# Kernel tuning notes

Measured on AMD Instinct MI355X. Metric: run time of the kernel, lower is better.

Reference implementation:

```python
import jax, jax.numpy as jnp
import numpy as np

NEG_SLOPE = 0.2
RECON_W = 0.1
BN_EPS = 1e-5


def gat_conv(x, edge_index, W, a_src, a_dst, b):
    """PyG-style GATConv (eval mode, add_self_loops=True, concat heads).
    x: [N, F_in], W: [F_in, H*C], a_src/a_dst: [H, C], b: [H*C]."""
    N = x.shape[0]
    H, C = a_src.shape
    h = (x @ W).reshape(N, H, C)                      # [N,H,C]
    loop = jnp.arange(N, dtype=edge_index.dtype)
    src = jnp.concatenate([edge_index[0], loop])
    dst = jnp.concatenate([edge_index[1], loop])
    alpha_src = jnp.sum(h * a_src, axis=-1)           # [N,H]
    alpha_dst = jnp.sum(h * a_dst, axis=-1)           # [N,H]
    e = jax.nn.leaky_relu(alpha_src[src] + alpha_dst[dst], NEG_SLOPE)  # [E,H]
    # segment softmax over incoming edges of each destination node
    m = jax.ops.segment_max(e, dst, num_segments=N)
    e = jnp.exp(e - m[dst])
    s = jax.ops.segment_sum(e, dst, num_segments=N)
    p = e / s[dst]                                    # [E,H]
    out = jax.ops.segment_sum(p[:, :, None] * h[src], dst, num_segments=N)  # [N,H,C]
    return out.reshape(N, H * C) + b


def setup_inputs() -> dict:
    key = jax.random.key(0)
    ks = jax.random.split(key, 24)
    N, E = 100000, 800000
    F_in, hid, heads, n_cls, ctx_d, expl_d = 128, 32, 4, 10, 6, 32
    HC = hid * heads  # 128
    g = lambda k, shp, sc=0.1: jax.random.normal(k, shp, dtype=jnp.float32) * sc
    return {
        "x": jax.random.normal(ks[0], (N, F_in), dtype=jnp.float32),
        "edge_index": jax.random.randint(ks[1], (2, E), 0, N, dtype=jnp.int32),
        "context": jax.random.normal(ks[2], (N, ctx_d), dtype=jnp.float32),
        # GATConv 1: F_in -> hid, heads
        "W1": g(ks[3], (F_in, HC)), "a_src1": g(ks[4], (heads, hid)),
        "a_dst1": g(ks[5], (heads, hid)), "b1": g(ks[6], (HC,)),
        # BatchNorm1d(HC), eval mode
        "bn_gamma": jnp.ones((HC,), jnp.float32), "bn_beta": g(ks[7], (HC,)),
        "bn_mean": g(ks[8], (HC,)), "bn_var": jax.random.uniform(ks[9], (HC,), jnp.float32, 0.5, 1.5),
        # GATConv 2: HC -> hid, 1 head
        "W2": g(ks[10], (HC, hid)), "a_src2": g(ks[11], (1, hid)),
        "a_dst2": g(ks[12], (1, hid)), "b2": g(ks[13], (hid,)),
        # Reasoner MLP: ctx_d -> hid -> expl_d
        "rw1": g(ks[14], (ctx_d, hid)), "rb1": g(ks[15], (hid,)),
        "rw2": g(ks[16], (hid, expl_d)), "rb2": g(ks[17], (expl_d,)),
        # Decoder: expl_d -> hid
        "dw": g(ks[18], (expl_d, hid)), "db": g(ks[19], (hid,)),
        # Classifier: hid -> n_cls
        "cw": g(ks[20], (hid, n_cls)), "cb": g(ks[21], (n_cls,)),
    }


def reference(x, edge_index, context, W1, a_src1, a_dst1, b1,
              bn_gamma, bn_beta, bn_mean, bn_var,
              W2, a_src2, a_dst2, b2, rw1, rb1, rw2, rb2, dw, db, cw, cb):
    # layer 1: GAT -> BN(eval) -> ELU (dropout inactive in eval)
    h = gat_conv(x, edge_index, W1, a_src1, a_dst1, b1)
    h = (h - bn_mean) * jax.lax.rsqrt(bn_var + BN_EPS) * bn_gamma + bn_beta
    h = jax.nn.elu(h)
    # layer 2: GAT (1 head)
    h = gat_conv(h, edge_index, W2, a_src2, a_dst2, b2)  # [N, hid]
    # reasoner + decoder
    expl = jnp.maximum(context @ rw1 + rb1, 0.0) @ rw2 + rb2   # [N, expl_d]
    recon = expl @ dw + db                                     # [N, hid]
    combined = h + RECON_W * recon
    logits = combined @ cw + cb
    return jax.nn.log_softmax(logits, axis=1), expl
```

## Files before the change

kernel.cpp:

```cpp
#include <hip/hip_runtime.h>
#include <hip/hip_bf16.h>
#include <math.h>

#define NEG_SLOPE 0.2f
#define RECON_W 0.1f
#define BN_EPS 1e-5f
#define CAP 64
#define NB_SCAT 256

typedef __attribute__((ext_vector_type(8))) short short8;
typedef __attribute__((ext_vector_type(4))) float f32x4;

__device__ __forceinline__ float lrelu(float v) {
    return (v >= 0.f) ? v : NEG_SLOPE * v;
}
__device__ __forceinline__ unsigned short f2bf(float f) {
    unsigned int u = __float_as_uint(f);
    u = (u + 0x7fffu + ((u >> 16) & 1u)) >> 16;
    return (unsigned short)u;
}
__device__ __forceinline__ float bf2f(unsigned short u) {
    return __uint_as_float(((unsigned int)u) << 16);
}
__device__ __forceinline__ unsigned int pack2bf(float a, float b) {
    return (unsigned int)f2bf(a) | ((unsigned int)f2bf(b) << 16);
}
__device__ __forceinline__ void unpack2(unsigned int u, float& a, float& b) {
    a = bf2f((unsigned short)u);
    b = bf2f((unsigned short)(u >> 16));
}

__global__ __launch_bounds__(256) void prep_kernel(
    const float* __restrict__ W1, const float* __restrict__ W2,
    const float* __restrict__ b1, const float* __restrict__ g,
    const float* __restrict__ be, const float* __restrict__ m, const float* __restrict__ v,
    unsigned short* __restrict__ w1t, unsigned short* __restrict__ w2t,
    float* __restrict__ bnsc, float* __restrict__ bnsh) {
    int b = blockIdx.x, tid = threadIdx.x;
    if (b < 64) {
        int e = b * 256 + tid;
        w1t[e] = f2bf(W1[(e & 127) * 128 + (e >> 7)]);
    } else {
        #pragma unroll
        for (int it = 0; it < 16; it++) {
            int e = it * 256 + tid;
            w2t[e] = f2bf(W2[(e & 127) * 32 + (e >> 7)]);
        }
        if (tid < 128) {
            float s = rsqrtf(v[tid] + BN_EPS) * g[tid];
            bnsc[tid] = s;
            bnsh[tid] = (b1[tid] - m[tid]) * s + be[tid];
        }
    }
}

__global__ __launch_bounds__(256) void gemm1_mfma_kernel(
    const float* __restrict__ x, const unsigned short* __restrict__ w1t,
    const float* __restrict__ a_src, const float* __restrict__ a_dst,
    unsigned short* __restrict__ h1g, float* __restrict__ as1, float* __restrict__ ad1, int N,
    const int* __restrict__ esrc, const int* __restrict__ edst, int E,
    int* __restrict__ cnt, int* __restrict__ csrS) {
    __shared__ unsigned short sA[64 * 128];
    __shared__ unsigned short sBt[128 * 128];
    __shared__ float s_as[128], s_ad[128];
    int tid = threadIdx.x;

    if (blockIdx.x < NB_SCAT) {
        int stride = NB_SCAT * 256;
        #pragma unroll 2
        for (int e = blockIdx.x * 256 + tid; e < E; e += stride) {
            int s = esrc[e], d = edst[e];
            int pos = atomicAdd(&cnt[d], 1);
            if (pos < CAP) csrS[(size_t)d * CAP + pos] = s;
        }
        return;
    }
    int rowBase = (blockIdx.x - NB_SCAT) * 64;

    if (tid < 128) { s_as[tid] = a_src[tid]; s_ad[tid] = a_dst[tid]; }
    #pragma unroll
    for (int u = 0; u < 8; u++) {
        int f = tid + u * 256;
        int r = f >> 5, cg = f & 31;
        int gr = rowBase + r;
        float4 vv = make_float4(0.f, 0.f, 0.f, 0.f);
        if (gr < N) vv = *(const float4*)(x + (size_t)gr * 128 + cg * 4);
        uint2 pk;
        pk.x = pack2bf(vv.x, vv.y);
        pk.y = pack2bf(vv.z, vv.w);
        ((uint2*)sA)[f] = pk;
    }
    #pragma unroll
    for (int u = 0; u < 8; u++) {
        int f = tid + u * 256;
        ((uint4*)sBt)[f] = ((const uint4*)w1t)[f];
    }
    __syncthreads();

    int lane = tid & 63;
    int w = tid >> 6;
    int quad = lane >> 4;
    int m16 = lane & 15;

    f32x4 acc[8];
    #pragma unroll
    for (int t = 0; t < 8; t++) acc[t] = (f32x4){0.f, 0.f, 0.f, 0.f};

    #pragma unroll
    for (int kc = 0; kc < 4; kc++) {
        int k0 = kc * 32 + quad * 8;
        short8 af = *(const short8*)(sA + ((w * 16 + m16) * 128 + k0));
        #pragma unroll
        for (int t = 0; t < 8; t++) {
            short8 bf = *(const short8*)(sBt + ((t * 16 + m16) * 128 + k0));
            acc[t] = __builtin_amdgcn_mfma_f32_16x16x32_bf16(af, bf, acc[t], 0, 0, 0);
        }
    }

    #pragma unroll
    for (int t = 0; t < 8; t++) {
        #pragma unroll
        for (int r = 0; r < 4; r++) {
            int row = w * 16 + quad * 4 + r;
            int col = t * 16 + m16;
            sA[row * 128 + col] = f2bf(acc[t][r]);
        }
    }
    __syncthreads();
    #pragma unroll
    for (int u = 0; u < 8; u++) {
        int f = tid + u * 256;
        int r = f >> 5, cg = f & 31;
        int gr = rowBase + r;
        if (gr < N) *(uint2*)(h1g + (size_t)gr * 128 + cg * 4) = ((const uint2*)sA)[f];
    }
    {
        int row = tid >> 2, head = tid & 3;
        int gr = rowBase + row;
        if (gr < N) {
            const unsigned int* rowp = (const unsigned int*)(sA + row * 128);
            float ps = 0.f, pd = 0.f;
            #pragma unroll
            for (int j = 0; j < 16; j++) {
                float f0, f1;
                unpack2(rowp[head * 16 + j], f0, f1);
                int c = head * 32 + j * 2;
                ps = fmaf(f0, s_as[c], fmaf(f1, s_as[c + 1], ps));
                pd = fmaf(f0, s_ad[c], fmaf(f1, s_ad[c + 1], pd));
            }
            as1[gr * 4 + head] = ps;
            ad1[gr * 4 + head] = pd;
        }
    }
}

__global__ __launch_bounds__(256) void agg1_gemm2_kernel(
    const unsigned short* __restrict__ h1g,
    const float* __restrict__ as1, const float* __restrict__ ad1,
    const int* __restrict__ cnt, const int* __restrict__ csrS,
    const float* __restrict__ bnscale, const float* __restrict__ bnshift,
    const unsigned short* __restrict__ w2t,
    const float* __restrict__ a_src2, const float* __restrict__ a_dst2,
    unsigned short* __restrict__ h2g, float* __restrict__ as2, float* __restrict__ ad2,
    int N) {
    __shared__ int   sSrc[16][CAP + 1];
    __shared__ __align__(16) float sW[16][CAP + 1][4];
    __shared__ unsigned short sH[16 * 128];
    __shared__ float s_as[32], s_ad[32];
    int tid = threadIdx.x;
    int nid = tid >> 4;
    int l   = tid & 15;
    int n = blockIdx.x * 16 + nid;
    bool alive = (n < N);
    int total = 0;

    if (tid < 32) { s_as[tid] = a_src2[tid]; s_ad[tid] = a_dst2[tid]; }

    if (alive) {
        int deg = min(cnt[n], CAP);
        total = deg + 1;
        float4 ad4 = *(const float4*)(ad1 + (size_t)n * 4);
        for (int slot = l; slot < total; slot += 16) {
            int s = (slot < deg) ? csrS[(size_t)n * CAP + slot] : n;
            sSrc[nid][slot] = s;
            float4 a = *(const float4*)(as1 + (size_t)s * 4);
            float4 w4;
            w4.x = __expf(lrelu(a.x + ad4.x));
            w4.y = __expf(lrelu(a.y + ad4.y));
            w4.z = __expf(lrelu(a.z + ad4.z));
            w4.w = __expf(lrelu(a.w + ad4.w));
            *(float4*)(&sW[nid][slot][0]) = w4;
        }
    }
    __syncthreads();

    int hl = l >> 2;
    unsigned choff = (unsigned)(l << 3);
    const int* sS = sSrc[nid];
    const float* sWp = &sW[nid][0][0];

    float pa0 = 0.f, pa1 = 0.f, pa2 = 0.f, pa3 = 0.f;
    float pa4 = 0.f, pa5 = 0.f, pa6 = 0.f, pa7 = 0.f;
    float pb0 = 0.f, pb1 = 0.f, pb2 = 0.f, pb3 = 0.f;
    float pb4 = 0.f, pb5 = 0.f, pb6 = 0.f, pb7 = 0.f;
    float sa = 0.f, sb = 0.f;
    int j = 0;
    for (; j + 1 < total; j += 2) {
        int s0 = sS[j];
        int s1 = sS[j + 1];
        float w0 = sWp[(j << 2) + hl];
        float w1 = sWp[((j + 1) << 2) + hl];
        uint4 u0 = *(const uint4*)(h1g + (((unsigned)s0 << 7) + choff));
        uint4 u1 = *(const uint4*)(h1g + (((unsigned)s1 << 7) + choff));
        float f0, f1;
        unpack2(u0.x, f0, f1); pa0 = fmaf(w0, f0, pa0); pa1 = fmaf(w0, f1, pa1);
        unpack2(u0.y, f0, f1); pa2 = fmaf(w0, f0, pa2); pa3 = fmaf(w0, f1, pa3);
        unpack2(u0.z, f0, f1); pa4 = fmaf(w0, f0, pa4); pa5 = fmaf(w0, f1, pa5);
        unpack2(u0.w, f0, f1); pa6 = fmaf(w0, f0, pa6); pa7 = fmaf(w0, f1, pa7);
        sa += w0;
        unpack2(u1.x, f0, f1); pb0 = fmaf(w1, f0, pb0); pb1 = fmaf(w1, f1, pb1);
        unpack2(u1.y, f0, f1); pb2 = fmaf(w1, f0, pb2); pb3 = fmaf(w1, f1, pb3);
        unpack2(u1.z, f0, f1); pb4 = fmaf(w1, f0, pb4); pb5 = fmaf(w1, f1, pb5);
        unpack2(u1.w, f0, f1); pb6 = fmaf(w1, f0, pb6); pb7 = fmaf(w1, f1, pb7);
        sb += w1;
    }
    if (j < total) {
        int s0 = sS[j];
        float w0 = sWp[(j << 2) + hl];
        uint4 u0 = *(const uint4*)(h1g + (((unsigned)s0 << 7) + choff));
        float f0, f1;
        unpack2(u0.x, f0, f1); pa0 = fmaf(w0, f0, pa0); pa1 = fmaf(w0, f1, pa1);
        unpack2(u0.y, f0, f1); pa2 = fmaf(w0, f0, pa2); pa3 = fmaf(w0, f1, pa3);
        unpack2(u0.z, f0, f1); pa4 = fmaf(w0, f0, pa4); pa5 = fmaf(w0, f1, pa5);
        unpack2(u0.w, f0, f1); pa6 = fmaf(w0, f0, pa6); pa7 = fmaf(w0, f1, pa7);
        sa += w0;
    }
    uint4 pk = make_uint4(0u, 0u, 0u, 0u);
    if (alive) {
        float inv = 1.f / (sa + sb);
        float4 sc0 = *(const float4*)(bnscale + l * 8);
        float4 sc1 = *(const float4*)(bnscale + l * 8 + 4);
        float4 sh0 = *(const float4*)(bnshift + l * 8);
        float4 sh1 = *(const float4*)(bnshift + l * 8 + 4);
        float o0 = fmaf((pa0 + pb0) * inv, sc0.x, sh0.x);
        float o1 = fmaf((pa1 + pb1) * inv, sc0.y, sh0.y);
        float o2 = fmaf((pa2 + pb2) * inv, sc0.z, sh0.z);
        float o3 = fmaf((pa3 + pb3) * inv, sc0.w, sh0.w);
        float o4 = fmaf((pa4 + pb4) * inv, sc1.x, sh1.x);
        float o5 = fmaf((pa5 + pb5) * inv, sc1.y, sh1.y);
        float o6 = fmaf((pa6 + pb6) * inv, sc1.z, sh1.z);
        float o7 = fmaf((pa7 + pb7) * inv, sc1.w, sh1.w);
        o0 = (o0 > 0.f) ? o0 : expm1f(o0);
        o1 = (o1 > 0.f) ? o1 : expm1f(o1);
        o2 = (o2 > 0.f) ? o2 : expm1f(o2);
        o3 = (o3 > 0.f) ? o3 : expm1f(o3);
        o4 = (o4 > 0.f) ? o4 : expm1f(o4);
        o5 = (o5 > 0.f) ? o5 : expm1f(o5);
        o6 = (o6 > 0.f) ? o6 : expm1f(o6);
        o7 = (o7 > 0.f) ? o7 : expm1f(o7);
        pk.x = pack2bf(o0, o1);
        pk.y = pack2bf(o2, o3);
        pk.z = pack2bf(o4, o5);
        pk.w = pack2bf(o6, o7);
    }
    *(uint4*)(sH + nid * 128 + l * 8) = pk;
    __syncthreads();

    unsigned short* sBt = (unsigned short*)&sW[0][0][0];
    unsigned short* sC  = sBt + 32 * 128;
    #pragma unroll
    for (int u = 0; u < 2; u++) ((uint4*)sBt)[tid + u * 256] = ((const uint4*)w2t)[tid + u * 256];
    __syncthreads();

    if (tid < 64) {
        int quad = tid >> 4, m16 = tid & 15;
        f32x4 acc2[2];
        acc2[0] = (f32x4){0.f, 0.f, 0.f, 0.f};
        acc2[1] = (f32x4){0.f, 0.f, 0.f, 0.f};
        #pragma unroll
        for (int kc = 0; kc < 4; kc++) {
            int k0 = kc * 32 + quad * 8;
            short8 af = *(const short8*)(sH + m16 * 128 + k0);
            #pragma unroll
            for (int t = 0; t < 2; t++) {
                short8 bf = *(const short8*)(sBt + (t * 16 + m16) * 128 + k0);
                acc2[t] = __builtin_amdgcn_mfma_f32_16x16x32_bf16(af, bf, acc2[t], 0, 0, 0);
            }
        }
        #pragma unroll
        for (int t = 0; t < 2; t++) {
            #pragma unroll
            for (int r = 0; r < 4; r++) {
                sC[(quad * 4 + r) * 32 + t * 16 + m16] = f2bf(acc2[t][r]);
            }
        }
    }
    __syncthreads();

    if (tid < 64) {
        int row = tid >> 2, g = tid & 3;
        int gr = blockIdx.x * 16 + row;
        if (gr < N) *(uint4*)(h2g + (size_t)gr * 32 + g * 8) = ((const uint4*)sC)[tid];
    }
    if (tid >= 64 && tid < 80) {
        int row = tid - 64;
        int gr = blockIdx.x * 16 + row;
        if (gr < N) {
            const unsigned int* rowp = (const unsigned int*)(sC + row * 32);
            float ps = 0.f, pd = 0.f;
            #pragma unroll
            for (int jj = 0; jj < 16; jj++) {
                float f0, f1;
                unpack2(rowp[jj], f0, f1);
                ps = fmaf(f0, s_as[jj * 2], fmaf(f1, s_as[jj * 2 + 1], ps));
                pd = fmaf(f0, s_ad[jj * 2], fmaf(f1, s_ad[jj * 2 + 1], pd));
            }
            as2[gr] = ps;
            ad2[gr] = pd;
        }
    }
}

__global__ __launch_bounds__(256) void agg2_head_kernel(
    const unsigned short* __restrict__ h2g,
    const float* __restrict__ as2, const float* __restrict__ ad2,
    const int* __restrict__ cnt, const int* __restrict__ csrS,
    const float* __restrict__ b2, const float* __restrict__ context,
    const float* __restrict__ rw1, const float* __restrict__ rb1,
    const float* __restrict__ rw2, const float* __restrict__ rb2,
    const float* __restrict__ dw, const float* __restrict__ db,
    const float* __restrict__ cw, const float* __restrict__ cb,
    float* __restrict__ out_lsm, float* __restrict__ out_expl, int N) {
    __shared__ int   sSrc[32][CAP + 1];
    __shared__ __align__(16) float sW[32][CAP + 1];
    __shared__ float sHL[32][32];
    __shared__ float s_rw1[192], s_rw2[1024], s_dw[1024], s_cw[320];
    __shared__ float s_rb1[32], s_rb2[32], s_db[32], s_b2[32], s_cb[16];
    int tid = threadIdx.x;
    for (int i = tid; i < 1024; i += 256) { s_rw2[i] = rw2[i]; s_dw[i] = dw[i]; }
    for (int i = tid; i < 320; i += 256) s_cw[i] = cw[i];
    if (tid < 192) s_rw1[tid] = rw1[tid];
    if (tid < 32) { s_rb1[tid] = rb1[tid]; s_rb2[tid] = rb2[tid]; s_db[tid] = db[tid]; s_b2[tid] = b2[tid]; }
    if (tid < 10) s_cb[tid] = cb[tid];

    int nid = tid >> 3;
    int l   = tid & 7;
    int n = blockIdx.x * 32 + nid;
    bool alive = (n < N);
    int total = 0;

    if (alive) {
        int deg = min(cnt[n], CAP);
        total = deg + 1;
        float ad = ad2[n];
        for (int slot = l; slot < total; slot += 8) {
            int s = (slot < deg) ? csrS[(size_t)n * CAP + slot] : n;
            sSrc[nid][slot] = s;
            sW[nid][slot] = __expf(lrelu(as2[s] + ad));
        }
    }
    __syncthreads();

    unsigned choff = (unsigned)(l << 2);
    const int* sS = sSrc[nid];
    const float* sWp = &sW[nid][0];

    float a0a = 0.f, a1a = 0.f, a2a = 0.f, a3a = 0.f, sa = 0.f;
    float a0b = 0.f, a1b = 0.f, a2b = 0.f, a3b = 0.f, sb = 0.f;
    int j = 0;
    for (; j + 1 < total; j += 2) {
        int s0 = sS[j];
        int s1 = sS[j + 1];
        float w0 = sWp[j];
        float w1 = sWp[j + 1];
        uint2 u0 = *(const uint2*)(h2g + (((unsigned)s0 << 5) + choff));
        uint2 u1 = *(const uint2*)(h2g + (((unsigned)s1 << 5) + choff));
        float f0, f1;
        unpack2(u0.x, f0, f1); a0a = fmaf(w0, f0, a0a); a1a = fmaf(w0, f1, a1a);
        unpack2(u0.y, f0, f1); a2a = fmaf(w0, f0, a2a); a3a = fmaf(w0, f1, a3a);
        sa += w0;
        unpack2(u1.x, f0, f1); a0b = fmaf(w1, f0, a0b); a1b = fmaf(w1, f1, a1b);
        unpack2(u1.y, f0, f1); a2b = fmaf(w1, f0, a2b); a3b = fmaf(w1, f1, a3b);
        sb += w1;
    }
    if (j < total) {
        int s0 = sS[j];
        float w0 = sWp[j];
        uint2 u0 = *(const uint2*)(h2g + (((unsigned)s0 << 5) + choff));
        float f0, f1;
        unpack2(u0.x, f0, f1); a0a = fmaf(w0, f0, a0a); a1a = fmaf(w0, f1, a1a);
        unpack2(u0.y, f0, f1); a2a = fmaf(w0, f0, a2a); a3a = fmaf(w0, f1, a3a);
        sa += w0;
    }
    if (alive) {
        float inv = 1.f / (sa + sb);
        int c0 = l * 4;
        sHL[nid][c0 + 0] = (a0a + a0b) * inv + s_b2[c0 + 0];
        sHL[nid][c0 + 1] = (a1a + a1b) * inv + s_b2[c0 + 1];
        sHL[nid][c0 + 2] = (a2a + a2b) * inv + s_b2[c0 + 2];
        sHL[nid][c0 + 3] = (a3a + a3b) * inv + s_b2[c0 + 3];
    }
    __syncthreads();

    float* sEX = &sW[0][0];

    if (alive) {
        int c0 = l * 4;
        float ctxv[6];
        #pragma unroll
        for (int i = 0; i < 6; i++) ctxv[i] = context[(size_t)n * 6 + i];
        float t1[32];
        #pragma unroll
        for (int c = 0; c < 32; c++) t1[c] = s_rb1[c];
        #pragma unroll
        for (int i = 0; i < 6; i++) {
            float s = ctxv[i];
            #pragma unroll
            for (int c = 0; c < 32; c++) t1[c] = fmaf(s, s_rw1[i * 32 + c], t1[c]);
        }
        #pragma unroll
        for (int c = 0; c < 32; c++) t1[c] = fmaxf(t1[c], 0.f);

        float e0 = s_rb2[c0], e1 = s_rb2[c0 + 1], e2 = s_rb2[c0 + 2], e3 = s_rb2[c0 + 3];
        #pragma unroll
        for (int c = 0; c < 32; c++) {
            float s = t1[c];
            const float* rp = s_rw2 + c * 32 + c0;
            e0 = fmaf(s, rp[0], e0); e1 = fmaf(s, rp[1], e1);
            e2 = fmaf(s, rp[2], e2); e3 = fmaf(s, rp[3], e3);
        }
        *(float4*)(out_expl + (size_t)n * 32 + c0) = make_float4(e0, e1, e2, e3);
        sEX[nid * 32 + c0 + 0] = e0;
        sEX[nid * 32 + c0 + 1] = e1;
        sEX[nid * 32 + c0 + 2] = e2;
        sEX[nid * 32 + c0 + 3] = e3;
    }
    __syncthreads();

    if (alive) {
        int c0 = l * 4;
        float r0 = s_db[c0], r1 = s_db[c0 + 1], r2 = s_db[c0 + 2], r3 = s_db[c0 + 3];
        #pragma unroll
        for (int c = 0; c < 32; c++) {
            float s = sEX[nid * 32 + c];
            const float* dp = s_dw + c * 32 + c0;
            r0 = fmaf(s, dp[0], r0); r1 = fmaf(s, dp[1], r1);
            r2 = fmaf(s, dp[2], r2); r3 = fmaf(s, dp[3], r3);
        }
        float cmb[4];
        cmb[0] = sHL[nid][c0 + 0] + RECON_W * r0;
        cmb[1] = sHL[nid][c0 + 1] + RECON_W * r1;
        cmb[2] = sHL[nid][c0 + 2] + RECON_W * r2;
        cmb[3] = sHL[nid][c0 + 3] + RECON_W * r3;
        float lg[10];
        #pragma unroll
        for (int c = 0; c < 10; c++) lg[c] = 0.f;
        #pragma unroll
        for (int k = 0; k < 4; k++) {
            float s = cmb[k];
            const float* cp = s_cw + (c0 + k) * 10;
            #pragma unroll
            for (int c = 0; c < 10; c++) lg[c] = fmaf(s, cp[c], lg[c]);
        }
        #pragma unroll
        for (int m = 1; m < 8; m <<= 1) {
            #pragma unroll
            for (int c = 0; c < 10; c++) lg[c] += __shfl_xor(lg[c], m);
        }
        #pragma unroll
        for (int c = 0; c < 10; c++) lg[c] += s_cb[c];
        float mx = lg[0];
        #pragma unroll
        for (int c = 1; c < 10; c++) mx = fmaxf(mx, lg[c]);
        float se = 0.f;
        #pragma unroll
        for (int c = 0; c < 10; c++) se += expf(lg[c] - mx);
        float lse = mx + logf(se);
        out_lsm[(size_t)n * 10 + l] = lg[l] - lse;
        if (l < 2) out_lsm[(size_t)n * 10 + 8 + l] = lg[8 + l] - lse;
    }
}

extern "C" void kernel_launch(void* const* d_in, const int* in_sizes, int n_in,
                              void* d_out, int out_size, void* d_ws, size_t ws_size,
                              hipStream_t stream) {
    const float* x    = (const float*)d_in[0];
    const int* ei     = (const int*)d_in[1];
    const float* ctx  = (const float*)d_in[2];
    const float* W1   = (const float*)d_in[3];
    const float* a_s1 = (const float*)d_in[4];
    const float* a_d1 = (const float*)d_in[5];
    const float* b1   = (const float*)d_in[6];
    const float* bn_g = (const float*)d_in[7];
    const float* bn_b = (const float*)d_in[8];
    const float* bn_m = (const float*)d_in[9];
    const float* bn_v = (const float*)d_in[10];
    const float* W2   = (const float*)d_in[11];
    const float* a_s2 = (const float*)d_in[12];
    const float* a_d2 = (const float*)d_in[13];
    const float* b2   = (const float*)d_in[14];
    const float* rw1  = (const float*)d_in[15];
    const float* rb1  = (const float*)d_in[16];
    const float* rw2  = (const float*)d_in[17];
    const float* rb2  = (const float*)d_in[18];
    const float* dw   = (const float*)d_in[19];
    const float* db   = (const float*)d_in[20];
    const float* cw   = (const float*)d_in[21];
    const float* cb   = (const float*)d_in[22];

    int N = in_sizes[0] / 128;
    int E = in_sizes[1] / 2;
    const int* esrc = ei;
    const int* edst = ei + E;

    char* w = (char*)d_ws;
    auto alloc = [&](size_t bytes) {
        void* p = (void*)w;
        w += (bytes + 255) & ~(size_t)255;
        return p;
    };
    unsigned short* h1g = (unsigned short*)alloc((size_t)N * 128 * 2);
    unsigned short* h2g = (unsigned short*)alloc((size_t)N * 32 * 2);
    float* as1  = (float*)alloc((size_t)N * 4 * 4);
    float* ad1  = (float*)alloc((size_t)N * 4 * 4);
    float* as2  = (float*)alloc((size_t)N * 4);
    float* ad2  = (float*)alloc((size_t)N * 4);
    int* cnt    = (int*)alloc((size_t)N * 4);
    int* csrS   = (int*)alloc((size_t)N * CAP * 4);
    float* bnsc = (float*)alloc(128 * 4);
    float* bnsh = (float*)alloc(128 * 4);
    unsigned short* w1t = (unsigned short*)alloc(128 * 128 * 2);
    unsigned short* w2t = (unsigned short*)alloc(32 * 128 * 2);

    float* out0 = (float*)d_out;
    float* out1 = out0 + (size_t)N * 10;

    hipMemsetAsync(cnt, 0, (size_t)N * 4, stream);

    prep_kernel<<<65, 256, 0, stream>>>(W1, W2, b1, bn_g, bn_b, bn_m, bn_v,
                                        w1t, w2t, bnsc, bnsh);
    gemm1_mfma_kernel<<<NB_SCAT + (N + 63) / 64, 256, 0, stream>>>(
        x, w1t, a_s1, a_d1, h1g, as1, ad1, N, esrc, edst, E, cnt, csrS);
    agg1_gemm2_kernel<<<(N + 15) / 16, 256, 0, stream>>>(
        h1g, as1, ad1, cnt, csrS, bnsc, bnsh, w2t, a_s2, a_d2, h2g, as2, ad2, N);
    agg2_head_kernel<<<(N + 31) / 32, 256, 0, stream>>>(
        h2g, as2, ad2, cnt, csrS, b2, ctx, rw1, rb1, rw2, rb2,
        dw, db, cw, cb, out0, out1, N);
}
```

Before: 272.5 us.

## Fuse memset, weight prep, and GEMM1/scatter into one cooperative persistent kernel

Replaces the memset, the prep kernel and the GEMM1+edge-scatter kernel with one cooperative kernel. It zeroes the counts, converts the weights and computes the BN constants, then runs a grid-wide sync. After the sync, a quarter of the blocks do the edge scatter and the rest loop persistently over 64-row GEMM tiles. This removes two launches and their gaps, but adds a grid barrier and a smaller persistent grid. The GEMM blocks now load the W1 tile once and reuse it across tiles, though each block may get less latency hiding than the old oversubscribed launch.

```diff
diff --git a/kernel.cpp b/kernel.cpp
--- a/kernel.cpp
+++ b/kernel.cpp
@@ -1,12 +1,14 @@
 #include <hip/hip_runtime.h>
+#include <hip/hip_cooperative_groups.h>
 #include <hip/hip_bf16.h>
 #include <math.h>
+
+namespace cg = cooperative_groups;
 
 #define NEG_SLOPE 0.2f
 #define RECON_W 0.1f
 #define BN_EPS 1e-5f
 #define CAP 64
-#define NB_SCAT 256
 
 typedef __attribute__((ext_vector_type(8))) short short8;
 typedef __attribute__((ext_vector_type(4))) float f32x4;
@@ -30,33 +32,14 @@
     b = bf2f((unsigned short)(u >> 16));
 }
 
-__global__ __launch_bounds__(256) void prep_kernel(
+__global__ __launch_bounds__(256) void fused1_kernel(
+    const float* __restrict__ x,
     const float* __restrict__ W1, const float* __restrict__ W2,
-    const float* __restrict__ b1, const float* __restrict__ g,
-    const float* __restrict__ be, const float* __restrict__ m, const float* __restrict__ v,
+    const float* __restrict__ b1, const float* __restrict__ bn_g,
+    const float* __restrict__ bn_b, const float* __restrict__ bn_m, const float* __restrict__ bn_v,
+    const float* __restrict__ a_src, const float* __restrict__ a_dst,
     unsigned short* __restrict__ w1t, unsigned short* __restrict__ w2t,
-    float* __restrict__ bnsc, float* __restrict__ bnsh) {
-    int b = blockIdx.x, tid = threadIdx.x;
-    if (b < 64) {
-        int e = b * 256 + tid;
-        w1t[e] = f2bf(W1[(e & 127) * 128 + (e >> 7)]);
-    } else {
-        #pragma unroll
-        for (int it = 0; it < 16; it++) {
-            int e = it * 256 + tid;
-            w2t[e] = f2bf(W2[(e & 127) * 32 + (e >> 7)]);
-        }
-        if (tid < 128) {
-            float s = rsqrtf(v[tid] + BN_EPS) * g[tid];
-            bnsc[tid] = s;
-            bnsh[tid] = (b1[tid] - m[tid]) * s + be[tid];
-        }
-    }
-}
-
-__global__ __launch_bounds__(256) void gemm1_mfma_kernel(
-    const float* __restrict__ x, const unsigned short* __restrict__ w1t,
-    const float* __restrict__ a_src, const float* __restrict__ a_dst,
+    float* __restrict__ bnsc, float* __restrict__ bnsh,
     unsigned short* __restrict__ h1g, float* __restrict__ as1, float* __restrict__ ad1, int N,
     const int* __restrict__ esrc, const int* __restrict__ edst, int E,
     int* __restrict__ cnt, int* __restrict__ csrS) {
@@ -64,9 +47,22 @@
     __shared__ unsigned short sBt[128 * 128];
     __shared__ float s_as[128], s_ad[128];
     int tid = threadIdx.x;
-
-    if (blockIdx.x < NB_SCAT) {
-        int stride = NB_SCAT * 256;
+    int T = gridDim.x * 256;
+    int gtid = blockIdx.x * 256 + tid;
+
+    for (int i = gtid; i < N; i += T) cnt[i] = 0;
+    for (int i = gtid; i < 16384; i += T) w1t[i] = f2bf(W1[(i & 127) * 128 + (i >> 7)]);
+    for (int i = gtid; i < 4096; i += T) w2t[i] = f2bf(W2[(i & 127) * 32 + (i >> 7)]);
+    for (int i = gtid; i < 128; i += T) {
+        float s = rsqrtf(bn_v[i] + BN_EPS) * bn_g[i];
+        bnsc[i] = s;
+        bnsh[i] = (b1[i] - bn_m[i]) * s + bn_b[i];
+    }
+    cg::this_grid().sync();
+
+    int nbs = gridDim.x >> 2;
+    if ((int)blockIdx.x < nbs) {
+        int stride = nbs * 256;
         #pragma unroll 2
         for (int e = blockIdx.x * 256 + tid; e < E; e += stride) {
             int s = esrc[e], d = edst[e];
@@ -75,81 +71,85 @@
         }
         return;
     }
-    int rowBase = (blockIdx.x - NB_SCAT) * 64;
 
     if (tid < 128) { s_as[tid] = a_src[tid]; s_ad[tid] = a_dst[tid]; }
     #pragma unroll
     for (int u = 0; u < 8; u++) {
         int f = tid + u * 256;
-        int r = f >> 5, cg = f & 31;
-        int gr = rowBase + r;
-        float4 vv = make_float4(0.f, 0.f, 0.f, 0.f);
-        if (gr < N) vv = *(const float4*)(x + (size_t)gr * 128 + cg * 4);
-        uint2 pk;
-        pk.x = pack2bf(vv.x, vv.y);
-        pk.y = pack2bf(vv.z, vv.w);
-        ((uint2*)sA)[f] = pk;
-    }
-    #pragma unroll
-    for (int u = 0; u < 8; u++) {
-        int f = tid + u * 256;
         ((uint4*)sBt)[f] = ((const uint4*)w1t)[f];
     }
-    __syncthreads();
 
     int lane = tid & 63;
     int w = tid >> 6;
     int quad = lane >> 4;
     int m16 = lane & 15;
-
-    f32x4 acc[8];
-    #pragma unroll
-    for (int t = 0; t < 8; t++) acc[t] = (f32x4){0.f, 0.f, 0.f, 0.f};
-
-    #pragma unroll
-    for (int kc = 0; kc < 4; kc++) {
-        int k0 = kc * 32 + quad * 8;
-        short8 af = *(const short8*)(sA + ((w * 16 + m16) * 128 + k0));
-        #pragma unroll
-        for (int t = 0; t < 8; t++) {
-            short8 bf = *(const short8*)(sBt + ((t * 16 + m16) * 128 + k0));
-            acc[t] = __builtin_amdgcn_mfma_f32_16x16x32_bf16(af, bf, acc[t], 0, 0, 0);
-        }
-    }
-
-    #pragma unroll
-    for (int t = 0; t < 8; t++) {
-        #pragma unroll
-        for (int r = 0; r < 4; r++) {
-            int row = w * 16 + quad * 4 + r;
-            int col = t * 16 + m16;
-            sA[row * 128 + col] = f2bf(acc[t][r]);
-        }
-    }
-    __syncthreads();
-    #pragma unroll
-    for (int u = 0; u < 8; u++) {
-        int f = tid + u * 256;
-        int r = f >> 5, cg = f & 31;
-        int gr = rowBase + r;
-        if (gr < N) *(uint2*)(h1g + (size_t)gr * 128 + cg * 4) = ((const uint2*)sA)[f];
-    }
-    {
-        int row = tid >> 2, head = tid & 3;
-        int gr = rowBase + row;
-        if (gr < N) {
-            const unsigned int* rowp = (const unsigned int*)(sA + row * 128);
-            float ps = 0.f, pd = 0.f;
-            #pragma unroll
-            for (int j = 0; j < 16; j++) {
-                float f0, f1;
-                unpack2(rowp[head * 16 + j], f0, f1);
-                int c = head * 32 + j * 2;
-                ps = fmaf(f0, s_as[c], fmaf(f1, s_as[c + 1], ps));
-                pd = fmaf(f0, s_ad[c], fmaf(f1, s_ad[c + 1], pd));
+    int nTiles = (N + 63) / 64;
+    int gstride = gridDim.x - nbs;
+
+    for (int t = (int)blockIdx.x - nbs; t < nTiles; t += gstride) {
+        __syncthreads();
+        int rowBase = t * 64;
+        #pragma unroll
+        for (int u = 0; u < 8; u++) {
+            int f = tid + u * 256;
+            int r = f >> 5, cg2 = f & 31;
+            int gr = rowBase + r;
+            float4 vv = make_float4(0.f, 0.f, 0.f, 0.f);
+            if (gr < N) vv = *(const float4*)(x + (size_t)gr * 128 + cg2 * 4);
+            uint2 pk;
+            pk.x = pack2bf(vv.x, vv.y);
+            pk.y = pack2bf(vv.z, vv.w);
+            ((uint2*)sA)[f] = pk;
+        }
+        __syncthreads();
+
+        f32x4 acc[8];
+        #pragma unroll
+        for (int tt = 0; tt < 8; tt++) acc[tt] = (f32x4){0.f, 0.f, 0.f, 0.f};
+        #pragma unroll
+        for (int kc = 0; kc < 4; kc++) {
+            int k0 = kc * 32 + quad * 8;
+            short8 af = *(const short8*)(sA + ((w * 16 + m16) * 128 + k0));
+            #pragma unroll
+            for (int tt = 0; tt < 8; tt++) {
+                short8 bf = *(const short8*)(sBt + ((tt * 16 + m16) * 128 + k0));
+                acc[tt] = __builtin_amdgcn_mfma_f32_16x16x32_bf16(af, bf, acc[tt], 0, 0, 0);
             }
-            as1[gr * 4 + head] = ps;
-            ad1[gr * 4 + head] = pd;
+        }
+        #pragma unroll
+        for (int tt = 0; tt < 8; tt++) {
+            #pragma unroll
+            for (int r = 0; r < 4; r++) {
+                int row = w * 16 + quad * 4 + r;
+                int col = tt * 16 + m16;
+                sA[row * 128 + col] = f2bf(acc[tt][r]);
+            }
+        }
+        __syncthreads();
+        #pragma unroll
+        for (int u = 0; u < 8; u++) {
+            int f = tid + u * 256;
+            int r = f >> 5, cg2 = f & 31;
+            int gr = rowBase + r;
+            if (gr < N) *(uint2*)(h1g + (size_t)gr * 128 + cg2 * 4) = ((const uint2*)sA)[f];
+        }
+        {
+            int row = tid >> 2, head = tid & 3;
+            int gr = rowBase + row;
+            if (gr < N) {
+                const unsigned int* rowp = (const unsigned int*)(sA + row * 128);
+                float ps = 0.f, pd = 0.f;
+                #pragma unroll
+                for (int j = 0; j < 16; j++) {
+                    float f0, f1;
+                    unpack2(rowp[head * 16 + j], f0, f1);
+                    int c = head * 32 + j * 2;
+                    ps = fmaf(f0, s_as[c], fmaf(f1, s_as[c + 1], ps));
+                    pd = fmaf(f0, s_ad[c], fmaf(f1, s_ad[c + 1], pd));
+                }
+                as1[gr * 4 + head] = ps;
+                ad1[gr * 4 + head] = pd;
+            }
         }
     }
 }
@@ -535,12 +535,26 @@
     float* out0 = (float*)d_out;
     float* out1 = out0 + (size_t)N * 10;
 
-    hipMemsetAsync(cnt, 0, (size_t)N * 4, stream);
-
-    prep_kernel<<<65, 256, 0, stream>>>(W1, W2, b1, bn_g, bn_b, bn_m, bn_v,
-                                        w1t, w2t, bnsc, bnsh);
-    gemm1_mfma_kernel<<<NB_SCAT + (N + 63) / 64, 256, 0, stream>>>(
-        x, w1t, a_s1, a_d1, h1g, as1, ad1, N, esrc, edst, E, cnt, csrS);
+    int maxBpc = 0;
+    if (hipOccupancyMaxActiveBlocksPerMultiprocessor(
+            &maxBpc, (const void*)fused1_kernel, 256, 0) != hipSuccess || maxBpc <= 0) {
+        maxBpc = 2;
+    }
+    if (maxBpc > 3) maxBpc = 3;
+    int coopGrid = maxBpc * 256;
+
+    void* args[] = {
+        (void*)&x, (void*)&W1, (void*)&W2,
+        (void*)&b1, (void*)&bn_g, (void*)&bn_b, (void*)&bn_m, (void*)&bn_v,
+        (void*)&a_s1, (void*)&a_d1,
+        (void*)&w1t, (void*)&w2t, (void*)&bnsc, (void*)&bnsh,
+        (void*)&h1g, (void*)&as1, (void*)&ad1, (void*)&N,
+        (void*)&esrc, (void*)&edst, (void*)&E,
+        (void*)&cnt, (void*)&csrS
+    };
+    hipLaunchCooperativeKernel((const void*)fused1_kernel, dim3(coopGrid), dim3(256),
+                               args, 0, stream);
+
     agg1_gemm2_kernel<<<(N + 15) / 16, 256, 0, stream>>>(
         h1g, as1, ad1, cnt, csrS, bnsc, bnsh, w2t, a_s2, a_d2, h2g, as2, ad2, N);
     agg2_head_kernel<<<(N + 31) / 32, 256, 0, stream>>>(
```

After: 365.1 us. 1.34x slower.
